# Kernel optimization log

Measured on AMD Instinct MI355X. Metric: run time of the kernel, lower is better.

The kernel has to match this reference:

```python
import jax, jax.numpy as jnp
import numpy as np

NEG_SLOPE = 0.2  # PyG GATConv default negative_slope


def _add_self_loops(edge_index, num_nodes):
    # PyG GATConv add_self_loops=True default
    loop = jnp.arange(num_nodes, dtype=edge_index.dtype)
    src = jnp.concatenate([edge_index[0], loop])
    dst = jnp.concatenate([edge_index[1], loop])
    return src, dst


def _gat_layer(x, src, dst, W, att_src, att_dst, bias, heads, out_ch):
    """One PyG-style GATConv layer (concat=True).
    x: [N, F_in]; W: [F_in, heads*out_ch]; att_*: [heads, out_ch]; bias: [heads*out_ch].
    """
    N = x.shape[0]
    h = (x @ W).reshape(N, heads, out_ch)               # [N, H, C]
    a_src = jnp.einsum('nhc,hc->nh', h, att_src)        # [N, H]
    a_dst = jnp.einsum('nhc,hc->nh', h, att_dst)        # [N, H]
    logits = jax.nn.leaky_relu(a_src[src] + a_dst[dst], NEG_SLOPE)  # [E, H]
    # segment softmax over destination neighborhoods
    m = jax.ops.segment_max(logits, dst, num_segments=N)            # [N, H]
    e = jnp.exp(logits - m[dst])                                     # [E, H]
    s = jax.ops.segment_sum(e, dst, num_segments=N)                  # [N, H]
    alpha = e / s[dst]                                               # [E, H]
    # scatter-aggregate weighted source features
    out = jax.ops.segment_sum(alpha[:, :, None] * h[src], dst, num_segments=N)  # [N, H, C]
    return out.reshape(N, heads * out_ch) + bias


def setup_inputs() -> dict:
    key = jax.random.key(0)
    ks = jax.random.split(key, 10)
    N, E = 50000, 800000
    F_in, HID, H, NC = 128, 64, 4, 10
    x = jax.random.normal(ks[0], (N, F_in), dtype=jnp.float32)
    edge_index = jax.random.randint(ks[1], (2, E), 0, N, dtype=jnp.int64)
    sc1 = 1.0 / np.sqrt(F_in)
    sc2 = 1.0 / np.sqrt(HID * H)
    return {
        'x': x,
        'edge_index': edge_index,
        'W1': jax.random.normal(ks[2], (F_in, H * HID), dtype=jnp.float32) * sc1,
        'att_src1': jax.random.normal(ks[3], (H, HID), dtype=jnp.float32) * sc1,
        'att_dst1': jax.random.normal(ks[4], (H, HID), dtype=jnp.float32) * sc1,
        'b1': jnp.zeros((H * HID,), dtype=jnp.float32),
        'W2': jax.random.normal(ks[5], (H * HID, NC), dtype=jnp.float32) * sc2,
        'att_src2': jax.random.normal(ks[6], (1, NC), dtype=jnp.float32) * sc2,
        'att_dst2': jax.random.normal(ks[7], (1, NC), dtype=jnp.float32) * sc2,
        'b2': jnp.zeros((NC,), dtype=jnp.float32),
    }


def reference(x, edge_index, W1, att_src1, att_dst1, b1, W2, att_src2, att_dst2, b2):
    N = x.shape[0]
    src, dst = _add_self_loops(edge_index, N)
    h = _gat_layer(x, src, dst, W1, att_src1, att_dst1, b1, heads=4, out_ch=64)
    h = jax.nn.elu(h)
    out = _gat_layer(h, src, dst, W2, att_src2, att_dst2, b2, heads=1, out_ch=10)
    return out
```

## Files before the change

### kernel.cpp

```cpp
#include <hip/hip_runtime.h>
#include <hip/hip_fp16.h>
#include <math.h>

#define NEG_SLOPE 0.2f
#define LOG2E 1.44269504088896f

#if __has_builtin(__builtin_amdgcn_exp2f)
#define EXP2(x) __builtin_amdgcn_exp2f(x)
#else
#define EXP2(x) exp2f(x)
#endif

typedef _Float16 half8 __attribute__((ext_vector_type(8)));
typedef float floatx4 __attribute__((ext_vector_type(4)));

__global__ __launch_bounds__(256) void prep1(const float* __restrict__ W1,
                                             half8* __restrict__ Bpack,
                                             int* __restrict__ zbuf, int N) {
  if (blockIdx.x < 16) {
    int tid = blockIdx.x * 256 + threadIdx.x;
    int l = tid & 63;
    int ksnt = tid >> 6;
    int ks = ksnt & 3;
    int nt = ksnt >> 2;
    int col = nt * 16 + (l & 15);
    int krow = ks * 32 + (l >> 4) * 8;
    half8 v;
#pragma unroll
    for (int j = 0; j < 8; j++) v[j] = (_Float16)W1[(krow + j) * 256 + col];
    Bpack[tid] = v;
  } else {
    int i = (blockIdx.x - 16) * 256 + threadIdx.x;
    if (i < N + 8192) zbuf[i] = 0;
  }
}

__global__ __launch_bounds__(256) void phase2(
    const float* __restrict__ x, const half8* __restrict__ Bpack,
    const float* __restrict__ att_s, const float* __restrict__ att_d,
    unsigned char* __restrict__ h1qh, float2* __restrict__ a1h,
    float* __restrict__ a1d,
    const int* __restrict__ dst, int* __restrict__ deg, int* __restrict__ rank,
    int N, int E, int gemmBlocks, int histBlocks) {
  if ((int)blockIdx.x >= gemmBlocks) {
    int b = blockIdx.x - gemmBlocks;
    for (int e = b * 256 + threadIdx.x; e < E; e += histBlocks * 256)
      rank[e] = atomicAdd(deg + dst[e], 1);
    return;
  }
  const int wave = threadIdx.x >> 6, lane = threadIdx.x & 63;
  const int quad = lane >> 4, li = lane & 15;
  const int n0 = (blockIdx.x * 4 + wave) * 16;
  if (n0 >= N) return;
  const size_t N64 = (size_t)N * 64;
  floatx4 acc[16];
#pragma unroll
  for (int t = 0; t < 16; t++) acc[t] = (floatx4){0.f, 0.f, 0.f, 0.f};
  const float* xrow = x + (size_t)(n0 + li) * 128;
#pragma unroll
  for (int ks = 0; ks < 4; ks++) {
    float4 xa = *(const float4*)(xrow + ks * 32 + quad * 8);
    float4 xb = *(const float4*)(xrow + ks * 32 + quad * 8 + 4);
    half8 a;
    a[0] = (_Float16)xa.x; a[1] = (_Float16)xa.y;
    a[2] = (_Float16)xa.z; a[3] = (_Float16)xa.w;
    a[4] = (_Float16)xb.x; a[5] = (_Float16)xb.y;
    a[6] = (_Float16)xb.z; a[7] = (_Float16)xb.w;
#pragma unroll
    for (int nt = 0; nt < 16; nt++) {
      half8 b = Bpack[(nt * 4 + ks) * 64 + lane];
      acc[nt] = __builtin_amdgcn_mfma_f32_16x16x32_f16(a, b, acc[nt], 0, 0, 0);
    }
  }
  float scv[4];
#pragma unroll
  for (int r = 0; r < 4; r++) {
    float m = 0.f;
#pragma unroll
    for (int nt = 0; nt < 16; nt++) m = fmaxf(m, fabsf(acc[nt][r]));
#pragma unroll
    for (int off = 8; off > 0; off >>= 1) m = fmaxf(m, __shfl_xor(m, off, 16));
    m = fmaxf(m, 1e-8f);
    float inv = 127.0f / m;
    scv[r] = m * (1.0f / 127.0f);
    int node = n0 + quad * 4 + r;
#pragma unroll
    for (int nt = 0; nt < 16; nt++) {
      h1qh[(size_t)(nt >> 2) * N64 + (size_t)node * 64 + (nt & 3) * 16 + li] =
          (unsigned char)(int)(fmaf(acc[nt][r], inv, 128.5f));
    }
  }
  float as_f[16], ad_f[16];
#pragma unroll
  for (int nt = 0; nt < 16; nt++) {
    as_f[nt] = att_s[nt * 16 + li];
    ad_f[nt] = att_d[nt * 16 + li];
  }
#pragma unroll
  for (int r = 0; r < 4; r++) {
    int node = n0 + quad * 4 + r;
#pragma unroll
    for (int h = 0; h < 4; h++) {
      float vs = 0.f, vd = 0.f;
#pragma unroll
      for (int ntl = 0; ntl < 4; ntl++) {
        int nt = h * 4 + ntl;
        vs = fmaf(acc[nt][r], as_f[nt], vs);
        vd = fmaf(acc[nt][r], ad_f[nt], vd);
      }
#pragma unroll
      for (int off = 8; off > 0; off >>= 1) {
        vs += __shfl_down(vs, off, 16);
        vd += __shfl_down(vd, off, 16);
      }
      if (li == 0) {
        a1h[(size_t)h * N + node] = make_float2(vs * LOG2E, scv[r]);
        a1d[node * 4 + h] = vd * LOG2E;
      }
    }
  }
}

__global__ void scan_local(const int* __restrict__ deg, int* __restrict__ excl,
                           int* __restrict__ bsum, int N) {
  __shared__ int s[256];
  int i = blockIdx.x * 256 + threadIdx.x;
  int v = (i < N) ? deg[i] + 1 : 0;
  s[threadIdx.x] = v;
  __syncthreads();
  for (int off = 1; off < 256; off <<= 1) {
    int t = (threadIdx.x >= off) ? s[threadIdx.x - off] : 0;
    __syncthreads();
    s[threadIdx.x] += t;
    __syncthreads();
  }
  if (i < N) excl[i] = s[threadIdx.x] - v;
  if (threadIdx.x == 255) bsum[blockIdx.x] = s[255];
}

__global__ __launch_bounds__(256) void histo(const int* __restrict__ deg,
                                             int* __restrict__ binCnt, int N) {
  __shared__ int h[256];
  h[threadIdx.x] = 0;
  __syncthreads();
  int i = blockIdx.x * 256 + threadIdx.x;
  if (i < N) atomicAdd(&h[min(deg[i], 255)], 1);
  __syncthreads();
  if (h[threadIdx.x] > 0) atomicAdd(binCnt + threadIdx.x * 16, h[threadIdx.x]);
}

__global__ void binscan(const int* __restrict__ binCnt, int* __restrict__ cursor) {
  __shared__ int s[256];
  int v = binCnt[threadIdx.x * 16];
  s[threadIdx.x] = v;
  __syncthreads();
  for (int off = 1; off < 256; off <<= 1) {
    int t = (threadIdx.x >= off) ? s[threadIdx.x - off] : 0;
    __syncthreads();
    s[threadIdx.x] += t;
    __syncthreads();
  }
  cursor[threadIdx.x * 16] = s[threadIdx.x] - v;
}

__global__ void scan_add2(const int* __restrict__ excl, const int* __restrict__ bsum,
                          int* __restrict__ rowptr, int* __restrict__ elist,
                          int N, int nb) {
  __shared__ int s[256];
  int v = (threadIdx.x < nb) ? bsum[threadIdx.x] : 0;
  s[threadIdx.x] = v;
  __syncthreads();
  for (int off = 1; off < 256; off <<= 1) {
    int t = (threadIdx.x >= off) ? s[threadIdx.x - off] : 0;
    __syncthreads();
    s[threadIdx.x] += t;
    __syncthreads();
  }
  __syncthreads();
  int base = (blockIdx.x > 0) ? s[blockIdx.x - 1] : 0;
  int i = blockIdx.x * 256 + threadIdx.x;
  if (i < N) {
    int r = excl[i] + base;
    rowptr[i] = r;
    elist[r] = i;
  }
  if (blockIdx.x == 0 && threadIdx.x == 0) rowptr[N] = s[nb - 1];
}

__global__ void scatter2(const int* __restrict__ src, const int* __restrict__ dst,
                         const int* __restrict__ rank, const int* __restrict__ rowptr,
                         int* __restrict__ elist, int E) {
  int e = blockIdx.x * 256 + threadIdx.x;
  if (e >= E) return;
  elist[rowptr[dst[e]] + 1 + rank[e]] = src[e];
}

__global__ __launch_bounds__(256) void place(const int* __restrict__ deg,
                                             int* __restrict__ cursor,
                                             int* __restrict__ perm, int N) {
  __shared__ int h[256];
  __shared__ int base[256];
  h[threadIdx.x] = 0;
  __syncthreads();
  int i = blockIdx.x * 256 + threadIdx.x;
  int b = 0, lr = 0;
  bool a = i < N;
  if (a) {
    b = min(deg[i], 255);
    lr = atomicAdd(&h[b], 1);
  }
  __syncthreads();
  if (h[threadIdx.x] > 0)
    base[threadIdx.x] = atomicAdd(cursor + threadIdx.x * 16, h[threadIdx.x]);
  __syncthreads();
  if (a) perm[base[b] + lr] = i;
}

__global__ __launch_bounds__(256) void agg1_heads(
    const int* __restrict__ rowptr, const int* __restrict__ elist,
    const int* __restrict__ perm,
    const unsigned char* __restrict__ h1qh, const float2* __restrict__ a1h,
    const float* __restrict__ a1d, const float* __restrict__ b1,
    const float* __restrict__ W2, float* __restrict__ phuf, int N) {
  __shared__ float w2s[256 * 11];
  const int t = threadIdx.x;
  for (int i = t; i < 2560; i += 256) {
    int ch = i / 10, jj = i - ch * 10;
    w2s[ch * 11 + jj] = W2[i];
  }

  const int wave = t >> 6, lane = t & 63;
  const int s = lane >> 3;
  const int k = lane & 7;
  const int xcd = blockIdx.x & 7;
  const int head = xcd >> 1, sub = xcd & 1;
  const int chunk = (blockIdx.x >> 3) * 2 + sub;
  const int gidx = chunk * 32 + wave * 8 + s;
  const bool act = gidx < N;
  const int n = act ? perm[gidx] : 0;
  const int row = act ? rowptr[n] : 0;
  const int en = act ? rowptr[n + 1] : 0;
  const float adh = act ? a1d[n * 4 + head] : 0.f;
  const float2* mh = a1h + (size_t)head * N;
  const unsigned char* hb = h1qh + (size_t)head * N * 64 + k * 8;

  float den = 0.f, T = 0.f;
  float acc[8];
#pragma unroll
  for (int u = 0; u < 8; u++) acc[u] = 0.f;

  int j = row;
  for (; j + 4 <= en; j += 4) {
    int ss[4];
    float2 mv[4];
    uint2 qv[4];
#pragma unroll
    for (int u = 0; u < 4; u++) ss[u] = elist[j + u];
#pragma unroll
    for (int u = 0; u < 4; u++) {
      mv[u] = mh[ss[u]];
      qv[u] = *(const uint2*)(hb + ((size_t)ss[u] << 6));
    }
#pragma unroll
    for (int u = 0; u < 4; u++) {
      float l = mv[u].x + adh;
      float e = EXP2(fmaxf(l, NEG_SLOPE * l));
      den += e;
      float se = e * mv[u].y;
      T += se;
      unsigned a = qv[u].x, b = qv[u].y;
      acc[0] = fmaf((float)(a & 0xffu), se, acc[0]);
      acc[1] = fmaf((float)((a >> 8) & 0xffu), se, acc[1]);
      acc[2] = fmaf((float)((a >> 16) & 0xffu), se, acc[2]);
      acc[3] = fmaf((float)(a >> 24), se, acc[3]);
      acc[4] = fmaf((float)(b & 0xffu), se, acc[4]);
      acc[5] = fmaf((float)((b >> 8) & 0xffu), se, acc[5]);
      acc[6] = fmaf((float)((b >> 16) & 0xffu), se, acc[6]);
      acc[7] = fmaf((float)(b >> 24), se, acc[7]);
    }
  }
  for (; j < en; j++) {
    int s0 = elist[j];
    float2 mv = mh[s0];
    uint2 q0 = *(const uint2*)(hb + ((size_t)s0 << 6));
    float l0 = mv.x + adh;
    float e0 = EXP2(fmaxf(l0, NEG_SLOPE * l0));
    den += e0;
    float se = e0 * mv.y;
    T += se;
    unsigned a = q0.x, b = q0.y;
    acc[0] = fmaf((float)(a & 0xffu), se, acc[0]);
    acc[1] = fmaf((float)((a >> 8) & 0xffu), se, acc[1]);
    acc[2] = fmaf((float)((a >> 16) & 0xffu), se, acc[2]);
    acc[3] = fmaf((float)(a >> 24), se, acc[3]);
    acc[4] = fmaf((float)(b & 0xffu), se, acc[4]);
    acc[5] = fmaf((float)((b >> 8) & 0xffu), se, acc[5]);
    acc[6] = fmaf((float)((b >> 16) & 0xffu), se, acc[6]);
    acc[7] = fmaf((float)(b >> 24), se, acc[7]);
  }

  __syncthreads();

  float bbv[8];
  {
    float4 b0 = *(const float4*)(b1 + head * 64 + k * 8);
    float4 b1v = *(const float4*)(b1 + head * 64 + k * 8 + 4);
    bbv[0] = b0.x; bbv[1] = b0.y; bbv[2] = b0.z; bbv[3] = b0.w;
    bbv[4] = b1v.x; bbv[5] = b1v.y; bbv[6] = b1v.z; bbv[7] = b1v.w;
  }
  float inv = act ? 1.0f / den : 0.f;
  float corr = 128.0f * T;
  float pv[10];
#pragma unroll
  for (int jj = 0; jj < 10; jj++) pv[jj] = 0.f;
#pragma unroll
  for (int u = 0; u < 8; u++) {
    float c = (acc[u] - corr) * inv + bbv[u];
    c = c > 0.f ? c : expm1f(c);
    const float* wrow = w2s + (head * 64 + k * 8 + u) * 11;
#pragma unroll
    for (int jj = 0; jj < 10; jj++) pv[jj] = fmaf(c, wrow[jj], pv[jj]);
  }
#pragma unroll
  for (int off = 4; off > 0; off >>= 1) {
#pragma unroll
    for (int jj = 0; jj < 10; jj++) pv[jj] += __shfl_down(pv[jj], off, 8);
  }
  if (act && k == 0) {
    float* pp = phuf + ((size_t)n * 4 + head) * 10;
#pragma unroll
    for (int jj = 0; jj < 10; jj++) pp[jj] = pv[jj];
  }
}

__global__ __launch_bounds__(256) void combine(
    const float* __restrict__ phuf, const float* __restrict__ as2,
    const float* __restrict__ ad2, __half* __restrict__ h2, int N) {
  int n = blockIdx.x * 256 + threadIdx.x;
  if (n >= N) return;
  const float* pp = phuf + (size_t)n * 40;
  float ds = 0.f, dd = 0.f;
#pragma unroll
  for (int jj = 0; jj < 10; jj++) {
    float p = pp[jj] + pp[10 + jj] + pp[20 + jj] + pp[30 + jj];
    h2[(size_t)n * 16 + jj] = __float2half(p);
    ds = fmaf(p, as2[jj], ds);
    dd = fmaf(p, ad2[jj], dd);
  }
  float* ft = (float*)(h2 + (size_t)n * 16);
  ft[5] = ds * LOG2E;
  ft[6] = dd * LOG2E;
}

__global__ __launch_bounds__(256) void agg2_csr(
    const int* __restrict__ rowptr, const int* __restrict__ elist,
    const __half* __restrict__ h2, const float* __restrict__ b2,
    float* __restrict__ out, int N) {
  int wave = threadIdx.x >> 6, lane = threadIdx.x & 63;
  int n = blockIdx.x * 4 + wave;
  if (n >= N) return;
  int row = rowptr[n];
  int deg = rowptr[n + 1] - row;
  const int* el = elist + row;
  const float* hf = (const float*)h2;
  float ad = hf[(size_t)n * 8 + 6];
  int g = lane / 5;
  int c2 = lane - g * 5;
  float den = 0.f, ax = 0.f, ay = 0.f;
  if (g < 12) {
    int jj = g;
    for (; jj + 12 < deg; jj += 24) {
      int sA = el[jj], sB = el[jj + 12];
      float lA = hf[(size_t)sA * 8 + 5] + ad;
      float lB = hf[(size_t)sB * 8 + 5] + ad;
      __half2 hA = *(const __half2*)(h2 + (size_t)sA * 16 + c2 * 2);
      __half2 hB = *(const __half2*)(h2 + (size_t)sB * 16 + c2 * 2);
      float eA = EXP2(fmaxf(lA, NEG_SLOPE * lA));
      float eB = EXP2(fmaxf(lB, NEG_SLOPE * lB));
      den += eA + eB;
      float2 fA = __half22float2(hA);
      float2 fB = __half22float2(hB);
      ax = fmaf(eA, fA.x, fmaf(eB, fB.x, ax));
      ay = fmaf(eA, fA.y, fmaf(eB, fB.y, ay));
    }
    for (; jj < deg; jj += 12) {
      int s = el[jj];
      float l = hf[(size_t)s * 8 + 5] + ad;
      __half2 hv = *(const __half2*)(h2 + (size_t)s * 16 + c2 * 2);
      float ev = EXP2(fmaxf(l, NEG_SLOPE * l));
      den += ev;
      float2 f = __half22float2(hv);
      ax = fmaf(ev, f.x, ax);
      ay = fmaf(ev, f.y, ay);
    }
  }
  ax += __shfl_down(ax, 30, 64);
  ay += __shfl_down(ay, 30, 64);
  den += __shfl_down(den, 30, 64);
  ax += __shfl_down(ax, 10, 64) + __shfl_down(ax, 20, 64);
  ay += __shfl_down(ay, 10, 64) + __shfl_down(ay, 20, 64);
  den += __shfl_down(den, 10, 64) + __shfl_down(den, 20, 64);
  ax += __shfl_down(ax, 5, 64);
  ay += __shfl_down(ay, 5, 64);
  den += __shfl_down(den, 5, 64);
  if (lane < 5) {
    float inv = 1.0f / den;
    float2 bb = *(const float2*)(b2 + lane * 2);
    float2 o = make_float2(fmaf(ax, inv, bb.x), fmaf(ay, inv, bb.y));
    *(float2*)(out + (size_t)n * 10 + lane * 2) = o;
  }
}

extern "C" void kernel_launch(void* const* d_in, const int* in_sizes, int n_in,
                              void* d_out, int out_size, void* d_ws, size_t ws_size,
                              hipStream_t stream) {
  const float* x = (const float*)d_in[0];
  const int* ei = (const int*)d_in[1];
  const float* W1 = (const float*)d_in[2];
  const float* as1 = (const float*)d_in[3];
  const float* ad1 = (const float*)d_in[4];
  const float* b1 = (const float*)d_in[5];
  const float* W2 = (const float*)d_in[6];
  const float* as2 = (const float*)d_in[7];
  const float* ad2 = (const float*)d_in[8];
  const float* b2 = (const float*)d_in[9];
  float* out = (float*)d_out;

  const int N = in_sizes[0] / 128;
  const int E = in_sizes[1] / 2;
  const int* srcp = ei;
  const int* dstp = ei + E;

  char* ws = (char*)d_ws;
  size_t off = 0;
  auto alloc = [&](size_t nbytes) {
    char* p = ws + off;
    off += (nbytes + 255) & ~(size_t)255;
    return p;
  };
  unsigned char* h1qh = (unsigned char*)alloc((size_t)N * 256);
  float2* a1h = (float2*)alloc((size_t)N * 4 * 8);
  half8* Bpack = (half8*)alloc((size_t)4096 * 16);
  float* a1d = (float*)alloc((size_t)N * 4 * 4);
  float* phuf = (float*)alloc((size_t)N * 40 * 4);
  __half* h2 = (__half*)alloc((size_t)N * 16 * 2);
  int* zbuf = (int*)alloc((size_t)(N + 8192) * 4);
  int* deg = zbuf;
  int* binCnt = zbuf + N;
  int* cursor = zbuf + N + 4096;
  int* excl = (int*)alloc((size_t)N * 4);
  int* bsum = (int*)alloc(256 * 4);
  int* rowptr = (int*)alloc((size_t)(N + 1) * 4);
  int* perm = (int*)alloc((size_t)N * 4);
  int* rank = (int*)alloc((size_t)E * 4);
  int* elist = (int*)alloc((size_t)(E + (size_t)N) * 4);

  const int nb = (N + 255) / 256;
  const int nbz = (N + 8192 + 255) / 256;
  const int gemmBlocks = (N / 16 + 3) / 4;
  const int histBlocks = 512;
  const int chunks = (N + 31) / 32;
  const int hgrid = ((chunks + 1) / 2) * 8;

  prep1<<<16 + nbz, 256, 0, stream>>>(W1, Bpack, zbuf, N);
  phase2<<<gemmBlocks + histBlocks, 256, 0, stream>>>(
      x, Bpack, as1, ad1, h1qh, a1h, a1d, dstp, deg, rank, N, E,
      gemmBlocks, histBlocks);
  scan_local<<<nb, 256, 0, stream>>>(deg, excl, bsum, N);
  histo<<<nb, 256, 0, stream>>>(deg, binCnt, N);
  binscan<<<1, 256, 0, stream>>>(binCnt, cursor);
  scan_add2<<<nb, 256, 0, stream>>>(excl, bsum, rowptr, elist, N, nb);
  scatter2<<<(E + 255) / 256, 256, 0, stream>>>(srcp, dstp, rank, rowptr, elist, E);
  place<<<nb, 256, 0, stream>>>(deg, cursor, perm, N);
  agg1_heads<<<hgrid, 256, 0, stream>>>(rowptr, elist, perm, h1qh, a1h, a1d,
                                        b1, W2, phuf, N);
  combine<<<(N + 255) / 256, 256, 0, stream>>>(phuf, as2, ad2, h2, N);
  agg2_csr<<<(N + 3) / 4, 256, 0, stream>>>(rowptr, elist, h2, b2, out, N);
}
```

Measured before the change: 256.5 us.

## Shrink edge list to 16-bit indices, fuse histogram into scan, precompute node descriptors

Stores CSR source indices as unsigned short instead of int, halving the edge-list traffic in both aggregation kernels. This relies on N fitting in 16 bits, which holds for the test size of 50000 but not for general graphs. It folds the degree histogram into the local scan kernel to drop one launch. It also adds a small kernel that packs row start, degree and node id into one int2, so agg1 loads one descriptor instead of chasing perm and then rowptr.

```diff
diff --git a/kernel.cpp b/kernel.cpp
--- a/kernel.cpp
+++ b/kernel.cpp
@@ -122,12 +122,16 @@
 }
 
 __global__ void scan_local(const int* __restrict__ deg, int* __restrict__ excl,
-                           int* __restrict__ bsum, int N) {
+                           int* __restrict__ bsum, int* __restrict__ binCnt, int N) {
   __shared__ int s[256];
+  __shared__ int hh[256];
+  hh[threadIdx.x] = 0;
   int i = blockIdx.x * 256 + threadIdx.x;
-  int v = (i < N) ? deg[i] + 1 : 0;
+  int d = (i < N) ? deg[i] : -1;
+  int v = (i < N) ? d + 1 : 0;
   s[threadIdx.x] = v;
   __syncthreads();
+  if (d >= 0) atomicAdd(&hh[min(d, 255)], 1);
   for (int off = 1; off < 256; off <<= 1) {
     int t = (threadIdx.x >= off) ? s[threadIdx.x - off] : 0;
     __syncthreads();
@@ -136,17 +140,8 @@
   }
   if (i < N) excl[i] = s[threadIdx.x] - v;
   if (threadIdx.x == 255) bsum[blockIdx.x] = s[255];
-}
-
-__global__ __launch_bounds__(256) void histo(const int* __restrict__ deg,
-                                             int* __restrict__ binCnt, int N) {
-  __shared__ int h[256];
-  h[threadIdx.x] = 0;
-  __syncthreads();
-  int i = blockIdx.x * 256 + threadIdx.x;
-  if (i < N) atomicAdd(&h[min(deg[i], 255)], 1);
-  __syncthreads();
-  if (h[threadIdx.x] > 0) atomicAdd(binCnt + threadIdx.x * 16, h[threadIdx.x]);
+  __syncthreads();
+  if (hh[threadIdx.x] > 0) atomicAdd(binCnt + threadIdx.x * 16, hh[threadIdx.x]);
 }
 
 __global__ void binscan(const int* __restrict__ binCnt, int* __restrict__ cursor) {
@@ -164,7 +159,7 @@
 }
 
 __global__ void scan_add2(const int* __restrict__ excl, const int* __restrict__ bsum,
-                          int* __restrict__ rowptr, int* __restrict__ elist,
+                          int* __restrict__ rowptr, unsigned short* __restrict__ elist,
                           int N, int nb) {
   __shared__ int s[256];
   int v = (threadIdx.x < nb) ? bsum[threadIdx.x] : 0;
@@ -182,17 +177,17 @@
   if (i < N) {
     int r = excl[i] + base;
     rowptr[i] = r;
-    elist[r] = i;
+    elist[r] = (unsigned short)i;
   }
   if (blockIdx.x == 0 && threadIdx.x == 0) rowptr[N] = s[nb - 1];
 }
 
 __global__ void scatter2(const int* __restrict__ src, const int* __restrict__ dst,
                          const int* __restrict__ rank, const int* __restrict__ rowptr,
-                         int* __restrict__ elist, int E) {
+                         unsigned short* __restrict__ elist, int E) {
   int e = blockIdx.x * 256 + threadIdx.x;
   if (e >= E) return;
-  elist[rowptr[dst[e]] + 1 + rank[e]] = src[e];
+  elist[rowptr[dst[e]] + 1 + rank[e]] = (unsigned short)src[e];
 }
 
 __global__ __launch_bounds__(256) void place(const int* __restrict__ deg,
@@ -216,9 +211,18 @@
   if (a) perm[base[b] + lr] = i;
 }
 
+__global__ void mkdesc(const int* __restrict__ perm, const int* __restrict__ rowptr,
+                       int2* __restrict__ ndesc, int N) {
+  int g = blockIdx.x * 256 + threadIdx.x;
+  if (g >= N) return;
+  int n = perm[g];
+  int row = rowptr[n];
+  int d = rowptr[n + 1] - row;
+  ndesc[g] = make_int2(row, (d << 16) | n);
+}
+
 __global__ __launch_bounds__(256) void agg1_heads(
-    const int* __restrict__ rowptr, const int* __restrict__ elist,
-    const int* __restrict__ perm,
+    const int2* __restrict__ ndesc, const unsigned short* __restrict__ elist,
     const unsigned char* __restrict__ h1qh, const float2* __restrict__ a1h,
     const float* __restrict__ a1d, const float* __restrict__ b1,
     const float* __restrict__ W2, float* __restrict__ phuf, int N) {
@@ -237,9 +241,10 @@
   const int chunk = (blockIdx.x >> 3) * 2 + sub;
   const int gidx = chunk * 32 + wave * 8 + s;
   const bool act = gidx < N;
-  const int n = act ? perm[gidx] : 0;
-  const int row = act ? rowptr[n] : 0;
-  const int en = act ? rowptr[n + 1] : 0;
+  int2 nd = act ? ndesc[gidx] : make_int2(0, 0);
+  const int n = nd.y & 0xFFFF;
+  const int row = nd.x;
+  const int en = row + (nd.y >> 16);
   const float adh = act ? a1d[n * 4 + head] : 0.f;
   const float2* mh = a1h + (size_t)head * N;
   const unsigned char* hb = h1qh + (size_t)head * N * 64 + k * 8;
@@ -353,7 +358,7 @@
 }
 
 __global__ __launch_bounds__(256) void agg2_csr(
-    const int* __restrict__ rowptr, const int* __restrict__ elist,
+    const int* __restrict__ rowptr, const unsigned short* __restrict__ elist,
     const __half* __restrict__ h2, const float* __restrict__ b2,
     float* __restrict__ out, int N) {
   int wave = threadIdx.x >> 6, lane = threadIdx.x & 63;
@@ -361,7 +366,7 @@
   if (n >= N) return;
   int row = rowptr[n];
   int deg = rowptr[n + 1] - row;
-  const int* el = elist + row;
+  const unsigned short* el = elist + row;
   const float* hf = (const float*)h2;
   float ad = hf[(size_t)n * 8 + 6];
   int g = lane / 5;
@@ -452,8 +457,9 @@
   int* bsum = (int*)alloc(256 * 4);
   int* rowptr = (int*)alloc((size_t)(N + 1) * 4);
   int* perm = (int*)alloc((size_t)N * 4);
+  int2* ndesc = (int2*)alloc((size_t)N * 8);
   int* rank = (int*)alloc((size_t)E * 4);
-  int* elist = (int*)alloc((size_t)(E + (size_t)N) * 4);
+  unsigned short* elist = (unsigned short*)alloc((size_t)(E + (size_t)N) * 2);
 
   const int nb = (N + 255) / 256;
   const int nbz = (N + 8192 + 255) / 256;
@@ -466,13 +472,13 @@
   phase2<<<gemmBlocks + histBlocks, 256, 0, stream>>>(
       x, Bpack, as1, ad1, h1qh, a1h, a1d, dstp, deg, rank, N, E,
       gemmBlocks, histBlocks);
-  scan_local<<<nb, 256, 0, stream>>>(deg, excl, bsum, N);
-  histo<<<nb, 256, 0, stream>>>(deg, binCnt, N);
+  scan_local<<<nb, 256, 0, stream>>>(deg, excl, bsum, binCnt, N);
   binscan<<<1, 256, 0, stream>>>(binCnt, cursor);
   scan_add2<<<nb, 256, 0, stream>>>(excl, bsum, rowptr, elist, N, nb);
   scatter2<<<(E + 255) / 256, 256, 0, stream>>>(srcp, dstp, rank, rowptr, elist, E);
   place<<<nb, 256, 0, stream>>>(deg, cursor, perm, N);
-  agg1_heads<<<hgrid, 256, 0, stream>>>(rowptr, elist, perm, h1qh, a1h, a1d,
+  mkdesc<<<nb, 256, 0, stream>>>(perm, rowptr, ndesc, N);
+  agg1_heads<<<hgrid, 256, 0, stream>>>(ndesc, elist, h1qh, a1h, a1d,
                                         b1, W2, phuf, N);
   combine<<<(N + 255) / 256, 256, 0, stream>>>(phuf, as2, ad2, h2, N);
   agg2_csr<<<(N + 3) / 4, 256, 0, stream>>>(rowptr, elist, h2, b2, out, N);
```

Result: no change. 253.0 us (-1.3%).
